# Kernel optimization log

Hardware: AMD Instinct MI355X
Metric: run time of the kernel (lower is better)

Reference implementation:

```python
import jax, jax.numpy as jnp
import numpy as np

N_NODES = 50000
N_EDGES = 1600000
N_GRAPHS = 512
NEG_SLOPE = 0.2


def _glorot(key, shape):
    fan_in, fan_out = shape[0], shape[-1]
    lim = jnp.sqrt(6.0 / (fan_in + fan_out))
    return jax.random.uniform(key, shape, jnp.float32, -lim, lim)


def setup_inputs() -> dict:
    key = jax.random.key(0)
    ks = jax.random.split(key, 12)
    x = jax.random.normal(ks[0], (N_NODES, 5), jnp.float32)
    edge_index = jax.random.randint(ks[1], (2, N_EDGES), 0, N_NODES, jnp.int64)
    batch = jnp.sort(jax.random.randint(ks[2], (N_NODES,), 0, N_GRAPHS, jnp.int64))
    # layer0: in=5 -> heads=4, out=16 (concat -> 64)
    W1l = _glorot(ks[3], (5, 64))
    W1r = _glorot(ks[4], (5, 64))
    att1 = _glorot(ks[5], (4, 16))
    b1 = jnp.zeros((64,), jnp.float32)
    # layer1: in=64 -> heads=1, out=64 (no concat)
    W2l = _glorot(ks[6], (64, 64))
    W2r = _glorot(ks[7], (64, 64))
    att2 = _glorot(ks[8], (1, 64))
    b2 = jnp.zeros((64,), jnp.float32)
    # predictor Linear(64, 1)
    Wp = _glorot(ks[9], (64, 1))
    bp = jnp.zeros((1,), jnp.float32)
    return {"x": x, "edge_index": edge_index, "batch": batch,
            "W1l": W1l, "W1r": W1r, "att1": att1, "b1": b1,
            "W2l": W2l, "W2r": W2r, "att2": att2, "b2": b2,
            "Wp": Wp, "bp": bp}


def _gatv2(x, src, dst, Wl, Wr, att, b, heads, dim, concat):
    n = x.shape[0]
    xl = (x @ Wl).reshape(n, heads, dim)  # source transform
    xr = (x @ Wr).reshape(n, heads, dim)  # target transform
    s = jax.nn.leaky_relu(xl[src] + xr[dst], NEG_SLOPE)      # [E,H,D]
    e = jnp.einsum('ehd,hd->eh', s, att)                      # [E,H]
    m = jax.ops.segment_max(e, dst, num_segments=n)           # segment softmax
    p = jnp.exp(e - m[dst])
    denom = jax.ops.segment_sum(p, dst, num_segments=n) + 1e-16
    alpha = p / denom[dst]                                    # [E,H]
    out = jax.ops.segment_sum(xl[src] * alpha[..., None], dst, num_segments=n)
    out = out.reshape(n, heads * dim) if concat else out.mean(axis=1)
    return out + b


def reference(x, edge_index, batch, W1l, W1r, att1, b1, W2l, W2r, att2, b2, Wp, bp):
    n = x.shape[0]
    # PyG GATv2Conv default add_self_loops=True
    loop = jnp.arange(n, dtype=edge_index.dtype)
    src = jnp.concatenate([edge_index[0], loop])
    dst = jnp.concatenate([edge_index[1], loop])
    h = _gatv2(x, src, dst, W1l, W1r, att1, b1, heads=4, dim=16, concat=True)
    h = jax.nn.relu(h)  # dropout is identity at eval
    h = _gatv2(h, src, dst, W2l, W2r, att2, b2, heads=1, dim=64, concat=False)
    h = jax.nn.relu(h)
    # global_mean_pool over graph ids
    sums = jax.ops.segment_sum(h, batch, num_segments=N_GRAPHS)
    cnt = jax.ops.segment_sum(jnp.ones((n,), h.dtype), batch, num_segments=N_GRAPHS)
    pooled = sums / jnp.maximum(cnt, 1.0)[:, None]
    return (pooled @ Wp + bp).squeeze(-1)
```

## Files before the change

kernel.cpp:

```cpp
#include <hip/hip_runtime.h>
#include <hip/hip_fp16.h>
#include <math.h>

#define NEG_SLOPE 0.2f
#define BUCKET 96

__device__ __forceinline__ float lrelu(float x) { return fmaxf(x, NEG_SLOPE * x); }

template <int CTRL>
__device__ __forceinline__ float dpp_add(float x) {
    int t = __builtin_amdgcn_update_dpp(0, __float_as_int(x), CTRL, 0xF, 0xF, false);
    return x + __int_as_float(t);
}

__device__ __forceinline__ float red8(float x) {
    x = dpp_add<0xB1>(x);
    x = dpp_add<0x4E>(x);
    x = dpp_add<0x141>(x);
    return x;
}

__device__ __forceinline__ float red32(float x) {
    x = red8(x);
    x = dpp_add<0x140>(x);
    x += __shfl_xor(x, 16, 64);
    return x;
}

__global__ void k_scatter(const int* __restrict__ ei, int* __restrict__ cnt,
                          int* __restrict__ ssrc, int E, int ET, int n, int nsub) {
    int part = blockIdx.x & 7;
    int sub  = blockIdx.x >> 3;
    int lo = (int)(((long long)part * n) >> 3);
    int hi = (int)(((long long)(part + 1) * n) >> 3);
    int stride = nsub * blockDim.x;
    for (int e = sub * blockDim.x + threadIdx.x; e < ET; e += stride) {
        int src, dst;
        if (e < E) { src = ei[e]; dst = ei[E + e]; } else { src = dst = e - E; }
        if (dst >= lo && dst < hi) {
            int pos = atomicAdd(&cnt[dst], 1);
            if (pos < BUCKET) ssrc[dst * BUCKET + pos] = src;
        }
    }
}

__global__ void k_t1(const float* __restrict__ x,
                     const float* __restrict__ W1l, const float* __restrict__ W1r,
                     __half* __restrict__ xl, float* __restrict__ xr, int n) {
    __shared__ float sWl[5 * 64], sWr[5 * 64];
    int t = threadIdx.x;
    for (int i = t; i < 5 * 64; i += blockDim.x) { sWl[i] = W1l[i]; sWr[i] = W1r[i]; }
    __syncthreads();
    int tid = blockIdx.x * blockDim.x + t;
    if (tid >= n * 64) return;
    int node = tid >> 6, j = tid & 63;
    const float* xp = x + node * 5;
    float x0 = xp[0], x1 = xp[1], x2 = xp[2], x3 = xp[3], x4 = xp[4];
    float al = x0 * sWl[j] + x1 * sWl[64 + j] + x2 * sWl[128 + j] + x3 * sWl[192 + j] + x4 * sWl[256 + j];
    float ar = x0 * sWr[j] + x1 * sWr[64 + j] + x2 * sWr[128 + j] + x3 * sWr[192 + j] + x4 * sWr[256 + j];
    xl[tid] = __float2half(al);
    xr[tid] = ar;
}

__global__ void __launch_bounds__(256, 8)
k_gat1(const int* __restrict__ ssrc, const int* __restrict__ deg,
       const __half* __restrict__ xl, const float* __restrict__ xr,
       const float* __restrict__ att1, const float* __restrict__ b1,
       const float* __restrict__ W2l, const float* __restrict__ W2r,
       __half* __restrict__ hl, float* __restrict__ hr, int n) {
    __shared__ float sh[4][64];
    int t = threadIdx.x;
    int wid = t >> 6, lane = t & 63;
    int node = __builtin_amdgcn_readfirstlane(blockIdx.x * 4 + wid);
    int half = lane >> 5, l31 = lane & 31;
    if (node < n) {
        float2 xrd  = *(const float2*)(xr + (size_t)node * 64 + 2 * l31);
        float2 attv = *(const float2*)(att1 + 2 * l31);
        float m = -INFINITY, den = 0.f, acc0 = 0.f, acc1 = 0.f;
        const int* bp_ = ssrc + (size_t)node * BUCKET;
        int end = deg[node]; if (end > BUCKET) end = BUCKET;
        int k = 0;
        for (; k + 15 < end; k += 16) {
            float2 a[8];
#pragma unroll
            for (int j = 0; j < 8; ++j) {
                int s0 = bp_[k + 2 * j], s1 = bp_[k + 2 * j + 1];
                int sj = half ? s1 : s0;
                a[j] = __half22float2(*(const __half2*)(xl + ((unsigned)sj << 6) + 2u * l31));
            }
            float s[8];
#pragma unroll
            for (int j = 0; j < 8; ++j)
                s[j] = lrelu(a[j].x + xrd.x) * attv.x + lrelu(a[j].y + xrd.y) * attv.y;
#pragma unroll
            for (int j = 0; j < 8; ++j) s[j] = red8(s[j]);
            float mb = fmaxf(fmaxf(fmaxf(s[0], s[1]), fmaxf(s[2], s[3])),
                             fmaxf(fmaxf(s[4], s[5]), fmaxf(s[6], s[7])));
            float mn = fmaxf(m, mb);
            float sc = __expf(m - mn);
            den *= sc; acc0 *= sc; acc1 *= sc;
#pragma unroll
            for (int j = 0; j < 8; ++j) {
                float p = __expf(s[j] - mn);
                den += p; acc0 += p * a[j].x; acc1 += p * a[j].y;
            }
            m = mn;
        }
        for (; k + 7 < end; k += 8) {
            float2 a[4];
#pragma unroll
            for (int j = 0; j < 4; ++j) {
                int s0 = bp_[k + 2 * j], s1 = bp_[k + 2 * j + 1];
                int sj = half ? s1 : s0;
                a[j] = __half22float2(*(const __half2*)(xl + ((unsigned)sj << 6) + 2u * l31));
            }
            float s[4];
#pragma unroll
            for (int j = 0; j < 4; ++j)
                s[j] = lrelu(a[j].x + xrd.x) * attv.x + lrelu(a[j].y + xrd.y) * attv.y;
#pragma unroll
            for (int j = 0; j < 4; ++j) s[j] = red8(s[j]);
            float mb = fmaxf(fmaxf(s[0], s[1]), fmaxf(s[2], s[3]));
            float mn = fmaxf(m, mb);
            float sc = __expf(m - mn);
            den *= sc; acc0 *= sc; acc1 *= sc;
#pragma unroll
            for (int j = 0; j < 4; ++j) {
                float p = __expf(s[j] - mn);
                den += p; acc0 += p * a[j].x; acc1 += p * a[j].y;
            }
            m = mn;
        }
        for (; k + 1 < end; k += 2) {
            int s0 = bp_[k], s1 = bp_[k + 1];
            int sj = half ? s1 : s0;
            float2 a = __half22float2(*(const __half2*)(xl + ((unsigned)sj << 6) + 2u * l31));
            float s = lrelu(a.x + xrd.x) * attv.x + lrelu(a.y + xrd.y) * attv.y;
            s = red8(s);
            float mn = fmaxf(m, s);
            float sc = __expf(m - mn);
            float p  = __expf(s - mn);
            den = den * sc + p;
            acc0 = acc0 * sc + p * a.x;
            acc1 = acc1 * sc + p * a.y;
            m = mn;
        }
        if (k < end) {
            int sj = bp_[k];
            float2 a = __half22float2(*(const __half2*)(xl + ((unsigned)sj << 6) + 2u * l31));
            float s = lrelu(a.x + xrd.x) * attv.x + lrelu(a.y + xrd.y) * attv.y;
            s = red8(s);
            if (half == 0) {
                float mn = fmaxf(m, s);
                float sc = __expf(m - mn);
                float p  = __expf(s - mn);
                den = den * sc + p;
                acc0 = acc0 * sc + p * a.x;
                acc1 = acc1 * sc + p * a.y;
                m = mn;
            }
        }
        float m_o  = __shfl_xor(m, 32, 64);
        float d_o  = __shfl_xor(den, 32, 64);
        float a0_o = __shfl_xor(acc0, 32, 64);
        float a1_o = __shfl_xor(acc1, 32, 64);
        float mf = fmaxf(m, m_o);
        float sc = __expf(m - mf), sco = __expf(m_o - mf);
        float denf = den * sc + d_o * sco + 1e-16f;
        float2 b = *(const float2*)(b1 + 2 * l31);
        float o0 = fmaxf((acc0 * sc + a0_o * sco) / denf + b.x, 0.f);
        float o1 = fmaxf((acc1 * sc + a1_o * sco) / denf + b.y, 0.f);
        if (half == 0) *(float2*)&sh[wid][2 * l31] = make_float2(o0, o1);
    }
    __syncthreads();
    if (node >= n) return;
    float accl = 0.f, accr = 0.f;
#pragma unroll 8
    for (int q = 0; q < 64; ++q) {
        float hv = sh[wid][q];
        accl += hv * W2l[q * 64 + lane];
        accr += hv * W2r[q * 64 + lane];
    }
    hl[(size_t)node * 64 + lane] = __float2half(accl);
    hr[(size_t)node * 64 + lane] = accr;
}

__global__ void __launch_bounds__(256, 8)
k_gat2(const int* __restrict__ ssrc, const int* __restrict__ deg,
       const __half* __restrict__ hl, const float* __restrict__ hr,
       const float* __restrict__ att2, const float* __restrict__ b2,
       const int* __restrict__ batch,
       float* __restrict__ pooled, float* __restrict__ cnt, int n) {
    int node = __builtin_amdgcn_readfirstlane((blockIdx.x * blockDim.x + threadIdx.x) >> 6);
    if (node >= n) return;
    int lane = threadIdx.x & 63;
    int half = lane >> 5, l31 = lane & 31;
    float2 hrd  = *(const float2*)(hr + (size_t)node * 64 + 2 * l31);
    float2 attv = *(const float2*)(att2 + 2 * l31);
    float m = -INFINITY, den = 0.f, acc0 = 0.f, acc1 = 0.f;
    const int* bp_ = ssrc + (size_t)node * BUCKET;
    int end = deg[node]; if (end > BUCKET) end = BUCKET;
    int k = 0;
    for (; k + 15 < end; k += 16) {
        float2 a[8];
#pragma unroll
        for (int j = 0; j < 8; ++j) {
            int s0 = bp_[k + 2 * j], s1 = bp_[k + 2 * j + 1];
            int sj = half ? s1 : s0;
            a[j] = __half22float2(*(const __half2*)(hl + ((unsigned)sj << 6) + 2u * l31));
        }
        float s[8];
#pragma unroll
        for (int j = 0; j < 8; ++j)
            s[j] = lrelu(a[j].x + hrd.x) * attv.x + lrelu(a[j].y + hrd.y) * attv.y;
#pragma unroll
        for (int j = 0; j < 8; ++j) s[j] = red32(s[j]);
        float mb = fmaxf(fmaxf(fmaxf(s[0], s[1]), fmaxf(s[2], s[3])),
                         fmaxf(fmaxf(s[4], s[5]), fmaxf(s[6], s[7])));
        float mn = fmaxf(m, mb);
        float sc = __expf(m - mn);
        den *= sc; acc0 *= sc; acc1 *= sc;
#pragma unroll
        for (int j = 0; j < 8; ++j) {
            float p = __expf(s[j] - mn);
            den += p; acc0 += p * a[j].x; acc1 += p * a[j].y;
        }
        m = mn;
    }
    for (; k + 7 < end; k += 8) {
        float2 a[4];
#pragma unroll
        for (int j = 0; j < 4; ++j) {
            int s0 = bp_[k + 2 * j], s1 = bp_[k + 2 * j + 1];
            int sj = half ? s1 : s0;
            a[j] = __half22float2(*(const __half2*)(hl + ((unsigned)sj << 6) + 2u * l31));
        }
        float s[4];
#pragma unroll
        for (int j = 0; j < 4; ++j)
            s[j] = lrelu(a[j].x + hrd.x) * attv.x + lrelu(a[j].y + hrd.y) * attv.y;
#pragma unroll
        for (int j = 0; j < 4; ++j) s[j] = red32(s[j]);
        float mb = fmaxf(fmaxf(s[0], s[1]), fmaxf(s[2], s[3]));
        float mn = fmaxf(m, mb);
        float sc = __expf(m - mn);
        den *= sc; acc0 *= sc; acc1 *= sc;
#pragma unroll
        for (int j = 0; j < 4; ++j) {
            float p = __expf(s[j] - mn);
            den += p; acc0 += p * a[j].x; acc1 += p * a[j].y;
        }
        m = mn;
    }
    for (; k + 1 < end; k += 2) {
        int s0 = bp_[k], s1 = bp_[k + 1];
        int sj = half ? s1 : s0;
        float2 a = __half22float2(*(const __half2*)(hl + ((unsigned)sj << 6) + 2u * l31));
        float s = lrelu(a.x + hrd.x) * attv.x + lrelu(a.y + hrd.y) * attv.y;
        s = red32(s);
        float mn = fmaxf(m, s);
        float sc = __expf(m - mn);
        float p  = __expf(s - mn);
        den = den * sc + p;
        acc0 = acc0 * sc + p * a.x;
        acc1 = acc1 * sc + p * a.y;
        m = mn;
    }
    if (k < end) {
        int sj = bp_[k];
        float2 a = __half22float2(*(const __half2*)(hl + ((unsigned)sj << 6) + 2u * l31));
        float s = lrelu(a.x + hrd.x) * attv.x + lrelu(a.y + hrd.y) * attv.y;
        s = red32(s);
        if (half == 0) {
            float mn = fmaxf(m, s);
            float sc = __expf(m - mn);
            float p  = __expf(s - mn);
            den = den * sc + p;
            acc0 = acc0 * sc + p * a.x;
            acc1 = acc1 * sc + p * a.y;
            m = mn;
        }
    }
    float m_o  = __shfl_xor(m, 32, 64);
    float d_o  = __shfl_xor(den, 32, 64);
    float a0_o = __shfl_xor(acc0, 32, 64);
    float a1_o = __shfl_xor(acc1, 32, 64);
    float mf = fmaxf(m, m_o);
    float sc = __expf(m - mf), sco = __expf(m_o - mf);
    float denf = den * sc + d_o * sco + 1e-16f;
    float2 b = *(const float2*)(b2 + 2 * l31);
    float o0 = fmaxf((acc0 * sc + a0_o * sco) / denf + b.x, 0.f);
    float o1 = fmaxf((acc1 * sc + a1_o * sco) / denf + b.y, 0.f);
    int g = batch[node];
    atomicAdd(&pooled[(size_t)g * 64 + 2 * l31 + half], half ? o1 : o0);
    if (lane == 0) atomicAdd(&cnt[g], 1.0f);
}

__global__ void k_predict(const float* __restrict__ pooled, const float* __restrict__ cnt,
                          const float* __restrict__ Wp, const float* __restrict__ bp,
                          float* __restrict__ out, int G) {
    int tid = blockIdx.x * blockDim.x + threadIdx.x;
    int g = tid >> 6;
    if (g >= G) return;
    int lane = threadIdx.x & 63;
    float c = cnt[g];
    if (c < 1.f) c = 1.f;
    float v = (pooled[(size_t)g * 64 + lane] / c) * Wp[lane];
#pragma unroll
    for (int off = 32; off > 0; off >>= 1) v += __shfl_down(v, off, 64);
    if (lane == 0) out[g] = v + bp[0];
}

extern "C" void kernel_launch(void* const* d_in, const int* in_sizes, int n_in,
                              void* d_out, int out_size, void* d_ws, size_t ws_size,
                              hipStream_t stream) {
    const float* x    = (const float*)d_in[0];
    const int*   ei   = (const int*)d_in[1];
    const int*   batch= (const int*)d_in[2];
    const float* W1l  = (const float*)d_in[3];
    const float* W1r  = (const float*)d_in[4];
    const float* att1 = (const float*)d_in[5];
    const float* b1   = (const float*)d_in[6];
    const float* W2l  = (const float*)d_in[7];
    const float* W2r  = (const float*)d_in[8];
    const float* att2 = (const float*)d_in[9];
    const float* b2   = (const float*)d_in[10];
    const float* Wp   = (const float*)d_in[11];
    const float* bp   = (const float*)d_in[12];
    float* out = (float*)d_out;

    const int n  = in_sizes[0] / 5;
    const int E  = in_sizes[1] / 2;
    const int ET = E + n;
    const int G  = out_size;

    char* ws = (char*)d_ws;
    size_t off = 0;
    auto alloc_b = [&](size_t bytes) { void* p = (void*)(ws + off); off += (bytes + 15) & ~15ull; return p; };
    __half* xl    = (__half*)alloc_b((size_t)n * 64 * 2);
    float*  xr    = (float*)alloc_b((size_t)n * 64 * 4);
    __half* hl    = (__half*)alloc_b((size_t)n * 64 * 2);
    float*  hr    = (float*)alloc_b((size_t)n * 64 * 4);
    float*  pooled= (float*)alloc_b((size_t)G * 64 * 4);
    float*  cntf  = (float*)alloc_b((size_t)G * 4);
    int*    deg   = (int*)alloc_b((size_t)n * 4);
    int*    ssrc  = (int*)alloc_b((size_t)n * BUCKET * 4);

    size_t zero_bytes = (size_t)((char*)deg - (char*)pooled) + (size_t)n * 4;
    (void)hipMemsetAsync(pooled, 0, zero_bytes, stream);

    const int B = 256;
    const int NSUB = 256;

    k_scatter<<<8 * NSUB, B, 0, stream>>>(ei, deg, ssrc, E, ET, n, NSUB);

    k_t1<<<(n * 64 + B - 1) / B, B, 0, stream>>>(x, W1l, W1r, xl, xr, n);

    k_gat1<<<(n + 3) / 4, B, 0, stream>>>(ssrc, deg, xl, xr, att1, b1, W2l, W2r, hl, hr, n);
    k_gat2<<<((size_t)n * 64 + B - 1) / B, B, 0, stream>>>(ssrc, deg, hl, hr, att2, b2, batch, pooled, cntf, n);
    k_predict<<<(G * 64 + B - 1) / B, B, 0, stream>>>(pooled, cntf, Wp, bp, out, G);
}
```

Baseline: 350.0 us.

## Recompute layer-1 source features from packed raw inputs instead of gathering xl

Layer 1 no longer materialises the 64-wide fp16 source transform xl. Instead it stores the 5 raw input features per node, padded to 8 halves (16 bytes), and each lane recomputes its two xl outputs from W1l held in registers after gathering them. This cuts the gather traffic per edge from 128 bytes to a 16-byte broadcast load, in exchange for extra FMAs and higher register pressure. The change also skips the src load for edges outside the block's partition in the scatter kernel, doubles the gat2 main unroll to 32 edges, and lowers launch bounds from 8 to 6 waves.

```diff
diff --git a/kernel.cpp b/kernel.cpp
--- a/kernel.cpp
+++ b/kernel.cpp
@@ -25,6 +25,16 @@
     x = dpp_add<0x140>(x);
     x += __shfl_xor(x, 16, 64);
     return x;
+}
+
+__device__ __forceinline__ float2 xl_of(float4 raw, const float2* wl) {
+    float2 x01 = __half22float2(*(__half2*)&raw.x);
+    float2 x23 = __half22float2(*(__half2*)&raw.y);
+    float2 x45 = __half22float2(*(__half2*)&raw.z);
+    float2 r;
+    r.x = x01.x * wl[0].x + x01.y * wl[1].x + x23.x * wl[2].x + x23.y * wl[3].x + x45.x * wl[4].x;
+    r.y = x01.x * wl[0].y + x01.y * wl[1].y + x23.x * wl[2].y + x23.y * wl[3].y + x45.x * wl[4].y;
+    return r;
 }
 
 __global__ void k_scatter(const int* __restrict__ ei, int* __restrict__ cnt,
@@ -35,9 +45,9 @@
     int hi = (int)(((long long)(part + 1) * n) >> 3);
     int stride = nsub * blockDim.x;
     for (int e = sub * blockDim.x + threadIdx.x; e < ET; e += stride) {
-        int src, dst;
-        if (e < E) { src = ei[e]; dst = ei[E + e]; } else { src = dst = e - E; }
+        int dst = (e < E) ? ei[E + e] : (e - E);
         if (dst >= lo && dst < hi) {
+            int src = (e < E) ? ei[e] : dst;
             int pos = atomicAdd(&cnt[dst], 1);
             if (pos < BUCKET) ssrc[dst * BUCKET + pos] = src;
         }
@@ -45,26 +55,29 @@
 }
 
 __global__ void k_t1(const float* __restrict__ x,
-                     const float* __restrict__ W1l, const float* __restrict__ W1r,
-                     __half* __restrict__ xl, float* __restrict__ xr, int n) {
-    __shared__ float sWl[5 * 64], sWr[5 * 64];
+                     const float* __restrict__ W1r,
+                     __half* __restrict__ xp, float* __restrict__ xr, int n) {
+    __shared__ float sWr[5 * 64];
     int t = threadIdx.x;
-    for (int i = t; i < 5 * 64; i += blockDim.x) { sWl[i] = W1l[i]; sWr[i] = W1r[i]; }
+    for (int i = t; i < 5 * 64; i += blockDim.x) sWr[i] = W1r[i];
     __syncthreads();
     int tid = blockIdx.x * blockDim.x + t;
     if (tid >= n * 64) return;
     int node = tid >> 6, j = tid & 63;
-    const float* xp = x + node * 5;
-    float x0 = xp[0], x1 = xp[1], x2 = xp[2], x3 = xp[3], x4 = xp[4];
-    float al = x0 * sWl[j] + x1 * sWl[64 + j] + x2 * sWl[128 + j] + x3 * sWl[192 + j] + x4 * sWl[256 + j];
+    const float* xq = x + node * 5;
+    float x0 = xq[0], x1 = xq[1], x2 = xq[2], x3 = xq[3], x4 = xq[4];
     float ar = x0 * sWr[j] + x1 * sWr[64 + j] + x2 * sWr[128 + j] + x3 * sWr[192 + j] + x4 * sWr[256 + j];
-    xl[tid] = __float2half(al);
     xr[tid] = ar;
-}
-
-__global__ void __launch_bounds__(256, 8)
+    if (j < 8) {
+        float v = (j < 5) ? xq[j] : 0.f;
+        xp[node * 8 + j] = __float2half(v);
+    }
+}
+
+__global__ void __launch_bounds__(256, 6)
 k_gat1(const int* __restrict__ ssrc, const int* __restrict__ deg,
-       const __half* __restrict__ xl, const float* __restrict__ xr,
+       const __half* __restrict__ xp, const float* __restrict__ xr,
+       const float* __restrict__ W1l,
        const float* __restrict__ att1, const float* __restrict__ b1,
        const float* __restrict__ W2l, const float* __restrict__ W2r,
        __half* __restrict__ hl, float* __restrict__ hr, int n) {
@@ -74,6 +87,9 @@
     int node = __builtin_amdgcn_readfirstlane(blockIdx.x * 4 + wid);
     int half = lane >> 5, l31 = lane & 31;
     if (node < n) {
+        float2 wl[5];
+#pragma unroll
+        for (int q = 0; q < 5; ++q) wl[q] = *(const float2*)(W1l + q * 64 + 2 * l31);
         float2 xrd  = *(const float2*)(xr + (size_t)node * 64 + 2 * l31);
         float2 attv = *(const float2*)(att1 + 2 * l31);
         float m = -INFINITY, den = 0.f, acc0 = 0.f, acc1 = 0.f;
@@ -81,17 +97,19 @@
         int end = deg[node]; if (end > BUCKET) end = BUCKET;
         int k = 0;
         for (; k + 15 < end; k += 16) {
-            float2 a[8];
+            float4 raw[8];
 #pragma unroll
             for (int j = 0; j < 8; ++j) {
                 int s0 = bp_[k + 2 * j], s1 = bp_[k + 2 * j + 1];
                 int sj = half ? s1 : s0;
-                a[j] = __half22float2(*(const __half2*)(xl + ((unsigned)sj << 6) + 2u * l31));
-            }
-            float s[8];
-#pragma unroll
-            for (int j = 0; j < 8; ++j)
+                raw[j] = *(const float4*)(xp + ((unsigned)sj << 3));
+            }
+            float2 a[8]; float s[8];
+#pragma unroll
+            for (int j = 0; j < 8; ++j) {
+                a[j] = xl_of(raw[j], wl);
                 s[j] = lrelu(a[j].x + xrd.x) * attv.x + lrelu(a[j].y + xrd.y) * attv.y;
+            }
 #pragma unroll
             for (int j = 0; j < 8; ++j) s[j] = red8(s[j]);
             float mb = fmaxf(fmaxf(fmaxf(s[0], s[1]), fmaxf(s[2], s[3])),
@@ -107,17 +125,19 @@
             m = mn;
         }
         for (; k + 7 < end; k += 8) {
-            float2 a[4];
+            float4 raw[4];
 #pragma unroll
             for (int j = 0; j < 4; ++j) {
                 int s0 = bp_[k + 2 * j], s1 = bp_[k + 2 * j + 1];
                 int sj = half ? s1 : s0;
-                a[j] = __half22float2(*(const __half2*)(xl + ((unsigned)sj << 6) + 2u * l31));
-            }
-            float s[4];
-#pragma unroll
-            for (int j = 0; j < 4; ++j)
+                raw[j] = *(const float4*)(xp + ((unsigned)sj << 3));
+            }
+            float2 a[4]; float s[4];
+#pragma unroll
+            for (int j = 0; j < 4; ++j) {
+                a[j] = xl_of(raw[j], wl);
                 s[j] = lrelu(a[j].x + xrd.x) * attv.x + lrelu(a[j].y + xrd.y) * attv.y;
+            }
 #pragma unroll
             for (int j = 0; j < 4; ++j) s[j] = red8(s[j]);
             float mb = fmaxf(fmaxf(s[0], s[1]), fmaxf(s[2], s[3]));
@@ -134,7 +154,7 @@
         for (; k + 1 < end; k += 2) {
             int s0 = bp_[k], s1 = bp_[k + 1];
             int sj = half ? s1 : s0;
-            float2 a = __half22float2(*(const __half2*)(xl + ((unsigned)sj << 6) + 2u * l31));
+            float2 a = xl_of(*(const float4*)(xp + ((unsigned)sj << 3)), wl);
             float s = lrelu(a.x + xrd.x) * attv.x + lrelu(a.y + xrd.y) * attv.y;
             s = red8(s);
             float mn = fmaxf(m, s);
@@ -147,7 +167,7 @@
         }
         if (k < end) {
             int sj = bp_[k];
-            float2 a = __half22float2(*(const __half2*)(xl + ((unsigned)sj << 6) + 2u * l31));
+            float2 a = xl_of(*(const float4*)(xp + ((unsigned)sj << 3)), wl);
             float s = lrelu(a.x + xrd.x) * attv.x + lrelu(a.y + xrd.y) * attv.y;
             s = red8(s);
             if (half == 0) {
@@ -185,7 +205,7 @@
     hr[(size_t)node * 64 + lane] = accr;
 }
 
-__global__ void __launch_bounds__(256, 8)
+__global__ void __launch_bounds__(256, 6)
 k_gat2(const int* __restrict__ ssrc, const int* __restrict__ deg,
        const __half* __restrict__ hl, const float* __restrict__ hr,
        const float* __restrict__ att2, const float* __restrict__ b2,
@@ -201,27 +221,28 @@
     const int* bp_ = ssrc + (size_t)node * BUCKET;
     int end = deg[node]; if (end > BUCKET) end = BUCKET;
     int k = 0;
-    for (; k + 15 < end; k += 16) {
-        float2 a[8];
-#pragma unroll
-        for (int j = 0; j < 8; ++j) {
+    for (; k + 31 < end; k += 32) {
+        float2 a[16];
+#pragma unroll
+        for (int j = 0; j < 16; ++j) {
             int s0 = bp_[k + 2 * j], s1 = bp_[k + 2 * j + 1];
             int sj = half ? s1 : s0;
             a[j] = __half22float2(*(const __half2*)(hl + ((unsigned)sj << 6) + 2u * l31));
         }
-        float s[8];
-#pragma unroll
-        for (int j = 0; j < 8; ++j)
+        float s[16];
+#pragma unroll
+        for (int j = 0; j < 16; ++j)
             s[j] = lrelu(a[j].x + hrd.x) * attv.x + lrelu(a[j].y + hrd.y) * attv.y;
 #pragma unroll
-        for (int j = 0; j < 8; ++j) s[j] = red32(s[j]);
-        float mb = fmaxf(fmaxf(fmaxf(s[0], s[1]), fmaxf(s[2], s[3])),
-                         fmaxf(fmaxf(s[4], s[5]), fmaxf(s[6], s[7])));
+        for (int j = 0; j < 16; ++j) s[j] = red32(s[j]);
+        float mb = s[0];
+#pragma unroll
+        for (int j = 1; j < 16; ++j) mb = fmaxf(mb, s[j]);
         float mn = fmaxf(m, mb);
         float sc = __expf(m - mn);
         den *= sc; acc0 *= sc; acc1 *= sc;
 #pragma unroll
-        for (int j = 0; j < 8; ++j) {
+        for (int j = 0; j < 16; ++j) {
             float p = __expf(s[j] - mn);
             den += p; acc0 += p * a[j].x; acc1 += p * a[j].y;
         }
@@ -337,7 +358,7 @@
     char* ws = (char*)d_ws;
     size_t off = 0;
     auto alloc_b = [&](size_t bytes) { void* p = (void*)(ws + off); off += (bytes + 15) & ~15ull; return p; };
-    __half* xl    = (__half*)alloc_b((size_t)n * 64 * 2);
+    __half* xp    = (__half*)alloc_b((size_t)n * 8 * 2);
     float*  xr    = (float*)alloc_b((size_t)n * 64 * 4);
     __half* hl    = (__half*)alloc_b((size_t)n * 64 * 2);
     float*  hr    = (float*)alloc_b((size_t)n * 64 * 4);
@@ -354,9 +375,9 @@
 
     k_scatter<<<8 * NSUB, B, 0, stream>>>(ei, deg, ssrc, E, ET, n, NSUB);
 
-    k_t1<<<(n * 64 + B - 1) / B, B, 0, stream>>>(x, W1l, W1r, xl, xr, n);
-
-    k_gat1<<<(n + 3) / 4, B, 0, stream>>>(ssrc, deg, xl, xr, att1, b1, W2l, W2r, hl, hr, n);
+    k_t1<<<(n * 64 + B - 1) / B, B, 0, stream>>>(x, W1r, xp, xr, n);
+
+    k_gat1<<<(n + 3) / 4, B, 0, stream>>>(ssrc, deg, xp, xr, W1l, att1, b1, W2l, W2r, hl, hr, n);
     k_gat2<<<((size_t)n * 64 + B - 1) / B, B, 0, stream>>>(ssrc, deg, hl, hr, att2, b2, batch, pooled, cntf, n);
     k_predict<<<(G * 64 + B - 1) / B, B, 0, stream>>>(pooled, cntf, Wp, bp, out, G);
 }
```

New measurement: 401.6 us. 14.7% more time.

## Process four edges per wavefront with 16-lane groups in GAT aggregation kernels

Applied to the files above, without the earlier changes.

Both GAT aggregation kernels now split each 64-lane wavefront into four 16-lane groups, each handling a separate edge with 8-byte half4 loads. Twice as many edges are in flight per iteration, and the per-edge attention reduction becomes shorter: 4 lanes via DPP in layer 1, 16 lanes in layer 2 with no cross-row shuffle. In exchange there are more accumulators, a two-step shuffle merge of softmax partials that guards against empty groups, and wasted lanes in the masked tail loop. The scatter kernel also defers loading the source index until the destination falls in the block's partition.

```diff
diff --git a/kernel.cpp b/kernel.cpp
--- a/kernel.cpp
+++ b/kernel.cpp
@@ -13,17 +13,16 @@
     return x + __int_as_float(t);
 }
 
-__device__ __forceinline__ float red8(float x) {
+__device__ __forceinline__ float red4(float x) {
     x = dpp_add<0xB1>(x);
     x = dpp_add<0x4E>(x);
+    return x;
+}
+
+__device__ __forceinline__ float red16(float x) {
+    x = red4(x);
     x = dpp_add<0x141>(x);
-    return x;
-}
-
-__device__ __forceinline__ float red32(float x) {
-    x = red8(x);
     x = dpp_add<0x140>(x);
-    x += __shfl_xor(x, 16, 64);
     return x;
 }
 
@@ -35,9 +34,9 @@
     int hi = (int)(((long long)(part + 1) * n) >> 3);
     int stride = nsub * blockDim.x;
     for (int e = sub * blockDim.x + threadIdx.x; e < ET; e += stride) {
-        int src, dst;
-        if (e < E) { src = ei[e]; dst = ei[E + e]; } else { src = dst = e - E; }
+        int dst = (e < E) ? ei[E + e] : (e - E);
         if (dst >= lo && dst < hi) {
+            int src = (e < E) ? ei[e] : dst;
             int pos = atomicAdd(&cnt[dst], 1);
             if (pos < BUCKET) ssrc[dst * BUCKET + pos] = src;
         }
@@ -62,6 +61,12 @@
     xr[tid] = ar;
 }
 
+__device__ __forceinline__ float4 h4_to_f4(uint2 r) {
+    float2 a01 = __half22float2(*(__half2*)&r.x);
+    float2 a23 = __half22float2(*(__half2*)&r.y);
+    return make_float4(a01.x, a01.y, a23.x, a23.y);
+}
+
 __global__ void __launch_bounds__(256, 8)
 k_gat1(const int* __restrict__ ssrc, const int* __restrict__ deg,
        const __half* __restrict__ xl, const float* __restrict__ xr,
@@ -72,114 +77,121 @@
     int t = threadIdx.x;
     int wid = t >> 6, lane = t & 63;
     int node = __builtin_amdgcn_readfirstlane(blockIdx.x * 4 + wid);
-    int half = lane >> 5, l31 = lane & 31;
+    int g = lane >> 4, q = lane & 15;
     if (node < n) {
-        float2 xrd  = *(const float2*)(xr + (size_t)node * 64 + 2 * l31);
-        float2 attv = *(const float2*)(att1 + 2 * l31);
-        float m = -INFINITY, den = 0.f, acc0 = 0.f, acc1 = 0.f;
+        float4 xrd  = *(const float4*)(xr + (size_t)node * 64 + 4 * q);
+        float4 attv = *(const float4*)(att1 + 4 * q);
+        float m = -INFINITY, den = 0.f;
+        float ac0 = 0.f, ac1 = 0.f, ac2 = 0.f, ac3 = 0.f;
         const int* bp_ = ssrc + (size_t)node * BUCKET;
         int end = deg[node]; if (end > BUCKET) end = BUCKET;
         int k = 0;
-        for (; k + 15 < end; k += 16) {
-            float2 a[8];
+        for (; k + 31 < end; k += 32) {
+            uint2 raw[8];
 #pragma unroll
             for (int j = 0; j < 8; ++j) {
-                int s0 = bp_[k + 2 * j], s1 = bp_[k + 2 * j + 1];
-                int sj = half ? s1 : s0;
-                a[j] = __half22float2(*(const __half2*)(xl + ((unsigned)sj << 6) + 2u * l31));
+                int sj = bp_[k + 4 * j + g];
+                raw[j] = *(const uint2*)(xl + ((unsigned)sj << 6) + 4u * q);
             }
             float s[8];
 #pragma unroll
-            for (int j = 0; j < 8; ++j)
-                s[j] = lrelu(a[j].x + xrd.x) * attv.x + lrelu(a[j].y + xrd.y) * attv.y;
-#pragma unroll
-            for (int j = 0; j < 8; ++j) s[j] = red8(s[j]);
-            float mb = fmaxf(fmaxf(fmaxf(s[0], s[1]), fmaxf(s[2], s[3])),
-                             fmaxf(fmaxf(s[4], s[5]), fmaxf(s[6], s[7])));
+            for (int j = 0; j < 8; ++j) {
+                float4 a = h4_to_f4(raw[j]);
+                s[j] = lrelu(a.x + xrd.x) * attv.x + lrelu(a.y + xrd.y) * attv.y
+                     + lrelu(a.z + xrd.z) * attv.z + lrelu(a.w + xrd.w) * attv.w;
+            }
+#pragma unroll
+            for (int j = 0; j < 8; ++j) s[j] = red4(s[j]);
+            float mb = s[0];
+#pragma unroll
+            for (int j = 1; j < 8; ++j) mb = fmaxf(mb, s[j]);
             float mn = fmaxf(m, mb);
             float sc = __expf(m - mn);
-            den *= sc; acc0 *= sc; acc1 *= sc;
+            den *= sc; ac0 *= sc; ac1 *= sc; ac2 *= sc; ac3 *= sc;
 #pragma unroll
             for (int j = 0; j < 8; ++j) {
                 float p = __expf(s[j] - mn);
-                den += p; acc0 += p * a[j].x; acc1 += p * a[j].y;
+                float4 a = h4_to_f4(raw[j]);
+                den += p; ac0 += p * a.x; ac1 += p * a.y; ac2 += p * a.z; ac3 += p * a.w;
             }
             m = mn;
         }
-        for (; k + 7 < end; k += 8) {
-            float2 a[4];
+        for (; k + 15 < end; k += 16) {
+            uint2 raw[4];
 #pragma unroll
             for (int j = 0; j < 4; ++j) {
-                int s0 = bp_[k + 2 * j], s1 = bp_[k + 2 * j + 1];
-                int sj = half ? s1 : s0;
-                a[j] = __half22float2(*(const __half2*)(xl + ((unsigned)sj << 6) + 2u * l31));
+                int sj = bp_[k + 4 * j + g];
+                raw[j] = *(const uint2*)(xl + ((unsigned)sj << 6) + 4u * q);
             }
             float s[4];
 #pragma unroll
-            for (int j = 0; j < 4; ++j)
-                s[j] = lrelu(a[j].x + xrd.x) * attv.x + lrelu(a[j].y + xrd.y) * attv.y;
-#pragma unroll
-            for (int j = 0; j < 4; ++j) s[j] = red8(s[j]);
+            for (int j = 0; j < 4; ++j) {
+                float4 a = h4_to_f4(raw[j]);
+                s[j] = lrelu(a.x + xrd.x) * attv.x + lrelu(a.y + xrd.y) * attv.y
+                     + lrelu(a.z + xrd.z) * attv.z + lrelu(a.w + xrd.w) * attv.w;
+            }
+#pragma unroll
+            for (int j = 0; j < 4; ++j) s[j] = red4(s[j]);
             float mb = fmaxf(fmaxf(s[0], s[1]), fmaxf(s[2], s[3]));
             float mn = fmaxf(m, mb);
             float sc = __expf(m - mn);
-            den *= sc; acc0 *= sc; acc1 *= sc;
+            den *= sc; ac0 *= sc; ac1 *= sc; ac2 *= sc; ac3 *= sc;
 #pragma unroll
             for (int j = 0; j < 4; ++j) {
                 float p = __expf(s[j] - mn);
-                den += p; acc0 += p * a[j].x; acc1 += p * a[j].y;
+                float4 a = h4_to_f4(raw[j]);
+                den += p; ac0 += p * a.x; ac1 += p * a.y; ac2 += p * a.z; ac3 += p * a.w;
             }
             m = mn;
         }
-        for (; k + 1 < end; k += 2) {
-            int s0 = bp_[k], s1 = bp_[k + 1];
-            int sj = half ? s1 : s0;
-            float2 a = __half22float2(*(const __half2*)(xl + ((unsigned)sj << 6) + 2u * l31));
-            float s = lrelu(a.x + xrd.x) * attv.x + lrelu(a.y + xrd.y) * attv.y;
-            s = red8(s);
-            float mn = fmaxf(m, s);
-            float sc = __expf(m - mn);
-            float p  = __expf(s - mn);
-            den = den * sc + p;
-            acc0 = acc0 * sc + p * a.x;
-            acc1 = acc1 * sc + p * a.y;
-            m = mn;
-        }
-        if (k < end) {
-            int sj = bp_[k];
-            float2 a = __half22float2(*(const __half2*)(xl + ((unsigned)sj << 6) + 2u * l31));
-            float s = lrelu(a.x + xrd.x) * attv.x + lrelu(a.y + xrd.y) * attv.y;
-            s = red8(s);
-            if (half == 0) {
+        for (; k < end; k += 4) {
+            int idx = k + g;
+            bool act = idx < end;
+            int sj = bp_[act ? idx : k];
+            float4 a = h4_to_f4(*(const uint2*)(xl + ((unsigned)sj << 6) + 4u * q));
+            float s = lrelu(a.x + xrd.x) * attv.x + lrelu(a.y + xrd.y) * attv.y
+                    + lrelu(a.z + xrd.z) * attv.z + lrelu(a.w + xrd.w) * attv.w;
+            s = red4(s);
+            if (act) {
                 float mn = fmaxf(m, s);
                 float sc = __expf(m - mn);
                 float p  = __expf(s - mn);
                 den = den * sc + p;
-                acc0 = acc0 * sc + p * a.x;
-                acc1 = acc1 * sc + p * a.y;
+                ac0 = ac0 * sc + p * a.x; ac1 = ac1 * sc + p * a.y;
+                ac2 = ac2 * sc + p * a.z; ac3 = ac3 * sc + p * a.w;
                 m = mn;
             }
         }
-        float m_o  = __shfl_xor(m, 32, 64);
-        float d_o  = __shfl_xor(den, 32, 64);
-        float a0_o = __shfl_xor(acc0, 32, 64);
-        float a1_o = __shfl_xor(acc1, 32, 64);
-        float mf = fmaxf(m, m_o);
-        float sc = __expf(m - mf), sco = __expf(m_o - mf);
-        float denf = den * sc + d_o * sco + 1e-16f;
-        float2 b = *(const float2*)(b1 + 2 * l31);
-        float o0 = fmaxf((acc0 * sc + a0_o * sco) / denf + b.x, 0.f);
-        float o1 = fmaxf((acc1 * sc + a1_o * sco) / denf + b.y, 0.f);
-        if (half == 0) *(float2*)&sh[wid][2 * l31] = make_float2(o0, o1);
+#pragma unroll
+        for (int step = 16; step <= 32; step <<= 1) {
+            float m_o = __shfl_xor(m, step, 64);
+            float d_o = __shfl_xor(den, step, 64);
+            float a0o = __shfl_xor(ac0, step, 64), a1o = __shfl_xor(ac1, step, 64);
+            float a2o = __shfl_xor(ac2, step, 64), a3o = __shfl_xor(ac3, step, 64);
+            float mf = fmaxf(m, m_o);
+            float sc  = (m   > -INFINITY) ? __expf(m   - mf) : 0.f;
+            float sco = (m_o > -INFINITY) ? __expf(m_o - mf) : 0.f;
+            den = den * sc + d_o * sco;
+            ac0 = ac0 * sc + a0o * sco; ac1 = ac1 * sc + a1o * sco;
+            ac2 = ac2 * sc + a2o * sco; ac3 = ac3 * sc + a3o * sco;
+            m = mf;
+        }
+        float denf = den + 1e-16f;
+        float4 bv = *(const float4*)(b1 + 4 * q);
+        float o0 = fmaxf(ac0 / denf + bv.x, 0.f);
+        float o1 = fmaxf(ac1 / denf + bv.y, 0.f);
+        float o2 = fmaxf(ac2 / denf + bv.z, 0.f);
+        float o3 = fmaxf(ac3 / denf + bv.w, 0.f);
+        if (g == 0) *(float4*)&sh[wid][4 * q] = make_float4(o0, o1, o2, o3);
     }
     __syncthreads();
     if (node >= n) return;
     float accl = 0.f, accr = 0.f;
 #pragma unroll 8
-    for (int q = 0; q < 64; ++q) {
-        float hv = sh[wid][q];
-        accl += hv * W2l[q * 64 + lane];
-        accr += hv * W2r[q * 64 + lane];
+    for (int r = 0; r < 64; ++r) {
+        float hv = sh[wid][r];
+        accl += hv * W2l[r * 64 + lane];
+        accr += hv * W2r[r * 64 + lane];
     }
     hl[(size_t)node * 64 + lane] = __float2half(accl);
     hr[(size_t)node * 64 + lane] = accr;
@@ -194,106 +206,114 @@
     int node = __builtin_amdgcn_readfirstlane((blockIdx.x * blockDim.x + threadIdx.x) >> 6);
     if (node >= n) return;
     int lane = threadIdx.x & 63;
-    int half = lane >> 5, l31 = lane & 31;
-    float2 hrd  = *(const float2*)(hr + (size_t)node * 64 + 2 * l31);
-    float2 attv = *(const float2*)(att2 + 2 * l31);
-    float m = -INFINITY, den = 0.f, acc0 = 0.f, acc1 = 0.f;
+    int g = lane >> 4, q = lane & 15;
+    float4 hrd  = *(const float4*)(hr + (size_t)node * 64 + 4 * q);
+    float4 attv = *(const float4*)(att2 + 4 * q);
+    float m = -INFINITY, den = 0.f;
+    float ac0 = 0.f, ac1 = 0.f, ac2 = 0.f, ac3 = 0.f;
     const int* bp_ = ssrc + (size_t)node * BUCKET;
     int end = deg[node]; if (end > BUCKET) end = BUCKET;
     int k = 0;
-    for (; k + 15 < end; k += 16) {
-        float2 a[8];
+    for (; k + 31 < end; k += 32) {
+        uint2 raw[8];
 #pragma unroll
         for (int j = 0; j < 8; ++j) {
-            int s0 = bp_[k + 2 * j], s1 = bp_[k + 2 * j + 1];
-            int sj = half ? s1 : s0;
-            a[j] = __half22float2(*(const __half2*)(hl + ((unsigned)sj << 6) + 2u * l31));
+            int sj = bp_[k + 4 * j + g];
+            raw[j] = *(const uint2*)(hl + ((unsigned)sj << 6) + 4u * q);
         }
         float s[8];
 #pragma unroll
-        for (int j = 0; j < 8; ++j)
-            s[j] = lrelu(a[j].x + hrd.x) * attv.x + lrelu(a[j].y + hrd.y) * attv.y;
-#pragma unroll
-        for (int j = 0; j < 8; ++j) s[j] = red32(s[j]);
-        float mb = fmaxf(fmaxf(fmaxf(s[0], s[1]), fmaxf(s[2], s[3])),
-                         fmaxf(fmaxf(s[4], s[5]), fmaxf(s[6], s[7])));
+        for (int j = 0; j < 8; ++j) {
+            float4 a = h4_to_f4(raw[j]);
+            s[j] = lrelu(a.x + hrd.x) * attv.x + lrelu(a.y + hrd.y) * attv.y
+                 + lrelu(a.z + hrd.z) * attv.z + lrelu(a.w + hrd.w) * attv.w;
+        }
+#pragma unroll
+        for (int j = 0; j < 8; ++j) s[j] = red16(s[j]);
+        float mb = s[0];
+#pragma unroll
+        for (int j = 1; j < 8; ++j) mb = fmaxf(mb, s[j]);
         float mn = fmaxf(m, mb);
         float sc = __expf(m - mn);
-        den *= sc; acc0 *= sc; acc1 *= sc;
+        den *= sc; ac0 *= sc; ac1 *= sc; ac2 *= sc; ac3 *= sc;
 #pragma unroll
         for (int j = 0; j < 8; ++j) {
             float p = __expf(s[j] - mn);
-            den += p; acc0 += p * a[j].x; acc1 += p * a[j].y;
+            float4 a = h4_to_f4(raw[j]);
+            den += p; ac0 += p * a.x; ac1 += p * a.y; ac2 += p * a.z; ac3 += p * a.w;
         }
         m = mn;
     }
-    for (; k + 7 < end; k += 8) {
-        float2 a[4];
+    for (; k + 15 < end; k += 16) {
+        uint2 raw[4];
 #pragma unroll
         for (int j = 0; j < 4; ++j) {
-            int s0 = bp_[k + 2 * j], s1 = bp_[k + 2 * j + 1];
-            int sj = half ? s1 : s0;
-            a[j] = __half22float2(*(const __half2*)(hl + ((unsigned)sj << 6) + 2u * l31));
+            int sj = bp_[k + 4 * j + g];
+            raw[j] = *(const uint2*)(hl + ((unsigned)sj << 6) + 4u * q);
         }
         float s[4];
 #pragma unroll
-        for (int j = 0; j < 4; ++j)
-            s[j] = lrelu(a[j].x + hrd.x) * attv.x + lrelu(a[j].y + hrd.y) * attv.y;
-#pragma unroll
-        for (int j = 0; j < 4; ++j) s[j] = red32(s[j]);
+        for (int j = 0; j < 4; ++j) {
+            float4 a = h4_to_f4(raw[j]);
+            s[j] = lrelu(a.x + hrd.x) * attv.x + lrelu(a.y + hrd.y) * attv.y
+                 + lrelu(a.z + hrd.z) * attv.z + lrelu(a.w + hrd.w) * attv.w;
+        }
+#pragma unroll
+        for (int j = 0; j < 4; ++j) s[j] = red16(s[j]);
         float mb = fmaxf(fmaxf(s[0], s[1]), fmaxf(s[2], s[3]));
         float mn = fmaxf(m, mb);
         float sc = __expf(m - mn);
-        den *= sc; acc0 *= sc; acc1 *= sc;
+        den *= sc; ac0 *= sc; ac1 *= sc; ac2 *= sc; ac3 *= sc;
 #pragma unroll
         for (int j = 0; j < 4; ++j) {
             float p = __expf(s[j] - mn);
-            den += p; acc0 += p * a[j].x; acc1 += p * a[j].y;
+            float4 a = h4_to_f4(raw[j]);
+            den += p; ac0 += p * a.x; ac1 += p * a.y; ac2 += p * a.z; ac3 += p * a.w;
         }
         m = mn;
     }
-    for (; k + 1 < end; k += 2) {
-        int s0 = bp_[k], s1 = bp_[k + 1];
-        int sj = half ? s1 : s0;
-        float2 a = __half22float2(*(const __half2*)(hl + ((unsigned)sj << 6) + 2u * l31));
-        float s = lrelu(a.x + hrd.x) * attv.x + lrelu(a.y + hrd.y) * attv.y;
-        s = red32(s);
-        float mn = fmaxf(m, s);
-        float sc = __expf(m - mn);
-        float p  = __expf(s - mn);
-        den = den * sc + p;
-        acc0 = acc0 * sc + p * a.x;
-        acc1 = acc1 * sc + p * a.y;
-        m = mn;
-    }
-    if (k < end) {
-        int sj = bp_[k];
-        float2 a = __half22float2(*(const __half2*)(hl + ((unsigned)sj << 6) + 2u * l31));
-        float s = lrelu(a.x + hrd.x) * attv.x + lrelu(a.y + hrd.y) * attv.y;
-        s = red32(s);
-        if (half == 0) {
+    for (; k < end; k += 4) {
+        int idx = k + g;
+        bool act = idx < end;
+        int sj = bp_[act ? idx : k];
+        float4 a = h4_to_f4(*(const uint2*)(hl + ((unsigned)sj << 6) + 4u * q));
+        float s = lrelu(a.x + hrd.x) * attv.x + lrelu(a.y + hrd.y) * attv.y
+                + lrelu(a.z + hrd.z) * attv.z + lrelu(a.w + hrd.w) * attv.w;
+        s = red16(s);
+        if (act) {
             float mn = fmaxf(m, s);
             float sc = __expf(m - mn);
             float p  = __expf(s - mn);
             den = den * sc + p;
-            acc0 = acc0 * sc + p * a.x;
-            acc1 = acc1 * sc + p * a.y;
+            ac0 = ac0 * sc + p * a.x; ac1 = ac1 * sc + p * a.y;
+            ac2 = ac2 * sc + p * a.z; ac3 = ac3 * sc + p * a.w;
             m = mn;
         }
     }
-    float m_o  = __shfl_xor(m, 32, 64);
-    float d_o  = __shfl_xor(den, 32, 64);
-    float a0_o = __shfl_xor(acc0, 32, 64);
-    float a1_o = __shfl_xor(acc1, 32, 64);
-    float mf = fmaxf(m, m_o);
-    float sc = __expf(m - mf), sco = __expf(m_o - mf);
-    float denf = den * sc + d_o * sco + 1e-16f;
-    float2 b = *(const float2*)(b2 + 2 * l31);
-    float o0 = fmaxf((acc0 * sc + a0_o * sco) / denf + b.x, 0.f);
-    float o1 = fmaxf((acc1 * sc + a1_o * sco) / denf + b.y, 0.f);
-    int g = batch[node];
-    atomicAdd(&pooled[(size_t)g * 64 + 2 * l31 + half], half ? o1 : o0);
-    if (lane == 0) atomicAdd(&cnt[g], 1.0f);
+#pragma unroll
+    for (int step = 16; step <= 32; step <<= 1) {
+        float m_o = __shfl_xor(m, step, 64);
+        float d_o = __shfl_xor(den, step, 64);
+        float a0o = __shfl_xor(ac0, step, 64), a1o = __shfl_xor(ac1, step, 64);
+        float a2o = __shfl_xor(ac2, step, 64), a3o = __shfl_xor(ac3, step, 64);
+        float mf = fmaxf(m, m_o);
+        float sc  = (m   > -INFINITY) ? __expf(m   - mf) : 0.f;
+        float sco = (m_o > -INFINITY) ? __expf(m_o - mf) : 0.f;
+        den = den * sc + d_o * sco;
+        ac0 = ac0 * sc + a0o * sco; ac1 = ac1 * sc + a1o * sco;
+        ac2 = ac2 * sc + a2o * sco; ac3 = ac3 * sc + a3o * sco;
+        m = mf;
+    }
+    float denf = den + 1e-16f;
+    float4 bv = *(const float4*)(b2 + 4 * q);
+    float o0 = fmaxf(ac0 / denf + bv.x, 0.f);
+    float o1 = fmaxf(ac1 / denf + bv.y, 0.f);
+    float o2 = fmaxf(ac2 / denf + bv.z, 0.f);
+    float o3 = fmaxf(ac3 / denf + bv.w, 0.f);
+    float og = (g == 0) ? o0 : (g == 1) ? o1 : (g == 2) ? o2 : o3;
+    int gid = batch[node];
+    atomicAdd(&pooled[(size_t)gid * 64 + 4 * q + g], og);
+    if (lane == 0) atomicAdd(&cnt[gid], 1.0f);
 }
 
 __global__ void k_predict(const float* __restrict__ pooled, const float* __restrict__ cnt,
```

Measured after the change: 390.2 us. +11.5%, slower.
